# Kernel tuning notes

Measured on AMD Instinct MI355X. Metric: run time of the kernel, lower is better.

## Reference

```python
import jax, jax.numpy as jnp
import numpy as np

N = 50000      # n_nodes
E = 800000     # n_edges (before self-loops)
IN = 256       # in_channels
MID = 512      # mid_channel
MID2 = MID // 2
OUT = 64       # out_channels


def setup_inputs() -> dict:
    key = jax.random.key(0)
    ks = jax.random.split(key, 16)
    def w(k, shape):
        fan_in = shape[0]
        return jax.random.normal(k, shape, jnp.float32) * (1.0 / np.sqrt(fan_in))
    return {
        "node_feature": jax.random.normal(ks[0], (N, IN), jnp.float32),
        "edge_index": jax.random.randint(ks[1], (2, E), 0, N, jnp.int32),
        # GCNConv weights (PyG convention: x @ W, bias added after aggregation)
        "Wg1": w(ks[2], (IN, MID)),   "bg1": jnp.zeros((MID,), jnp.float32),
        "Wg2": w(ks[3], (MID, MID2)), "bg2": jnp.zeros((MID2,), jnp.float32),
        "Wg3": w(ks[4], (MID2, OUT)), "bg3": jnp.zeros((OUT,), jnp.float32),
        # parallel Linear layers
        "Wl1": w(ks[5], (IN, MID)),   "bl1": jnp.zeros((MID,), jnp.float32),
        "Wl2": w(ks[6], (MID, MID2)), "bl2": jnp.zeros((MID2,), jnp.float32),
        "Wl3": w(ks[7], (MID2, OUT)), "bl3": jnp.zeros((OUT,), jnp.float32),
    }


def reference(node_feature, edge_index, Wg1, bg1, Wg2, bg2, Wg3, bg3,
              Wl1, bl1, Wl2, bl2, Wl3, bl3):
    n = node_feature.shape[0]
    # list_add_self_loops: append (i, i) for every node
    loops = jnp.arange(n, dtype=edge_index.dtype)
    src = jnp.concatenate([edge_index[0], loops])
    dst = jnp.concatenate([edge_index[1], loops])
    # symmetric GCN normalization: deg computed on graph with self-loops
    deg = jax.ops.segment_sum(jnp.ones_like(dst, jnp.float32), dst, num_segments=n)
    dis = jax.lax.rsqrt(jnp.maximum(deg, 1.0))  # deg >= 1 thanks to self-loops
    norm = dis[src] * dis[dst]                  # [E'] edge coefficients

    def gcn_conv(x, W, b):
        h = x @ W                                            # [N, F_out]
        msgs = h[src] * norm[:, None]                        # gather + scale
        return jax.ops.segment_sum(msgs, dst, num_segments=n) + b  # scatter-add

    h1 = jax.nn.elu(gcn_conv(node_feature, Wg1, bg1)) + node_feature @ Wl1 + bl1
    h2 = jax.nn.elu(gcn_conv(h1, Wg2, bg2)) + h1 @ Wl2 + bl2
    out = gcn_conv(h2, Wg3, bg3) + h2 @ Wl3 + bl3
    return out
```

## Files before the change

kernel.cpp:

```cpp
#include <hip/hip_runtime.h>
#include <hip/hip_bf16.h>
#include <math.h>

#define IN_CH  256
#define MID    512
#define MID2   256
#define OUT_CH 64

typedef __attribute__((ext_vector_type(8))) short s16x8;
typedef __attribute__((ext_vector_type(8))) unsigned short u16x8;
typedef __attribute__((ext_vector_type(4))) unsigned short u16x4;
typedef __attribute__((ext_vector_type(4))) float f32x4;


__global__ __launch_bounds__(256) void deg_kernel(const int* __restrict__ dst,
                                                  int* __restrict__ cnt, int E) {
  int stride = gridDim.x * blockDim.x;
  for (int e = blockIdx.x * blockDim.x + threadIdx.x; e < E; e += stride)
    atomicAdd(&cnt[dst[e]], 1);
}

__global__ __launch_bounds__(1024) void scan_dis_kernel(const int* __restrict__ cnt,
                                                        int* __restrict__ rowstart,
                                                        float* __restrict__ dis, int N) {
  __shared__ int part[1024];
  int t = threadIdx.x;
  int chunk = (N + 1023) >> 10;
  int lo = t * chunk;
  int hi = lo + chunk; if (hi > N) hi = N; if (lo > N) lo = N;
  int s = 0;
  for (int i = lo; i < hi; ++i) s += cnt[i] + 1;
  part[t] = s;
  __syncthreads();
  for (int off = 1; off < 1024; off <<= 1) {
    int v = (t >= off) ? part[t - off] : 0;
    __syncthreads();
    part[t] += v;
    __syncthreads();
  }
  int base = part[t] - s;
  for (int i = lo; i < hi; ++i) {
    int d = cnt[i] + 1;
    rowstart[i] = base;
    dis[i] = rsqrtf((float)d);
    base += d;
  }
  if (t == 1023) rowstart[N] = part[1023];
}

__global__ __launch_bounds__(256) void fill_adj_kernel(const int* __restrict__ src,
                                                       const int* __restrict__ dst,
                                                       const int* __restrict__ rowstart,
                                                       int* __restrict__ cnt2,
                                                       int* __restrict__ adj,
                                                       int E, int N) {
  int total = E + N;
  int stride = gridDim.x * blockDim.x;
  for (int e = blockIdx.x * blockDim.x + threadIdx.x; e < total; e += stride) {
    int s, d;
    if (e < E) { s = src[e]; d = dst[e]; }
    else       { s = d = e - E; }
    int pos = rowstart[d] + atomicAdd(&cnt2[d], 1);
    adj[pos] = s;
  }
}


__device__ inline unsigned bf16_rne(float v) {
  unsigned u = __float_as_uint(v);
  return (u + 0x7FFFu + ((u >> 16) & 1u)) >> 16;
}

__global__ __launch_bounds__(256) void wsplit_cat(const float* __restrict__ W,
                                                  unsigned short* __restrict__ Th,
                                                  unsigned short* __restrict__ Tl,
                                                  int K, int F, int noff) {
  int idx = blockIdx.x * 256 + threadIdx.x;
  if (idx >= K * F) return;
  int k = idx / F, n = idx - k * F;
  float v = W[idx];
  unsigned h = bf16_rne(v);
  float hf = __uint_as_float(h << 16);
  unsigned l = bf16_rne(v - hf);
  Th[(size_t)(noff + n) * K + k] = (unsigned short)h;
  Tl[(size_t)(noff + n) * K + k] = (unsigned short)l;
}

__global__ __launch_bounds__(256) void split_pair(const float* __restrict__ X,
                                                  unsigned short* __restrict__ Xh,
                                                  unsigned short* __restrict__ Xl,
                                                  int n8) {
  int i = blockIdx.x * 256 + threadIdx.x;
  if (i >= n8) return;
  const float4* xp = (const float4*)X + (size_t)i * 2;
  float4 a = xp[0], b = xp[1];
  float vv[8] = {a.x, a.y, a.z, a.w, b.x, b.y, b.z, b.w};
  u16x8 hv, lv;
  #pragma unroll
  for (int j = 0; j < 8; ++j) {
    unsigned h = bf16_rne(vv[j]);
    float hf = __uint_as_float(h << 16);
    unsigned l = bf16_rne(vv[j] - hf);
    hv[j] = (unsigned short)h;
    lv[j] = (unsigned short)l;
  }
  ((u16x8*)Xh)[i] = hv;
  ((u16x8*)Xl)[i] = lv;
}


template<int MODE>
__global__ __launch_bounds__(256, 2)
void gemm_ps(const unsigned short* __restrict__ Agh, const unsigned short* __restrict__ Agl,
             const unsigned short* __restrict__ Bgh, const unsigned short* __restrict__ Bgl,
             const float* __restrict__ bias,
             const float* __restrict__ C1r, float* __restrict__ C1w,
             unsigned short* __restrict__ O2h, unsigned short* __restrict__ O2l,
             float* __restrict__ O2f,
             int Nrows, int K, int F1) {
  __shared__ unsigned short lds[4 * 128 * 64];
  unsigned short* Ah = lds;
  unsigned short* Al = lds + 8192;
  unsigned short* Bh = lds + 16384;
  unsigned short* Bl = lds + 24576;

  const int tid  = threadIdx.x;
  const int lane = tid & 63;
  const int wid  = tid >> 6;
  const int wr = wid >> 1, wc = wid & 1;
  const int row0 = blockIdx.x * 128;
  const int col0 = blockIdx.y * 128;

  f32x4 acc[4][4] = {};

  const int sr    = tid >> 1;
  const int shalf = (tid & 1) << 5;
  int arow = row0 + sr; if (arow > Nrows - 1) arow = Nrows - 1;
  const unsigned short* Ahb = Agh + (size_t)arow * K + shalf;
  const unsigned short* Alb = Agl + (size_t)arow * K + shalf;
  const unsigned short* Bhb = Bgh + (size_t)(col0 + sr) * K + shalf;
  const unsigned short* Blb = Bgl + (size_t)(col0 + sr) * K + shalf;
  int wslot[4];
  #pragma unroll
  for (int i = 0; i < 4; ++i)
    wslot[i] = sr * 64 + ((((shalf >> 3) + i) ^ (sr & 7)) << 3);

  for (int k0 = 0; k0 < K; k0 += 64) {
    u16x8 rah[4], ral[4], rbh[4], rbl[4];
    #pragma unroll
    for (int i = 0; i < 4; ++i) rah[i] = *(const u16x8*)(Ahb + k0 + i * 8);
    #pragma unroll
    for (int i = 0; i < 4; ++i) ral[i] = *(const u16x8*)(Alb + k0 + i * 8);
    #pragma unroll
    for (int i = 0; i < 4; ++i) rbh[i] = *(const u16x8*)(Bhb + k0 + i * 8);
    #pragma unroll
    for (int i = 0; i < 4; ++i) rbl[i] = *(const u16x8*)(Blb + k0 + i * 8);

    __syncthreads();
    #pragma unroll
    for (int i = 0; i < 4; ++i) {
      *(u16x8*)(Ah + wslot[i]) = rah[i];
      *(u16x8*)(Al + wslot[i]) = ral[i];
      *(u16x8*)(Bh + wslot[i]) = rbh[i];
      *(u16x8*)(Bl + wslot[i]) = rbl[i];
    }
    __syncthreads();

    #pragma unroll
    for (int ks = 0; ks < 2; ++ks) {
      const int sw = ((((ks << 2) + (lane >> 4)) ^ (lane & 7)) << 3);
      s16x8 fah[4], fal[4], fbh[4], fbl[4];
      #pragma unroll
      for (int mi = 0; mi < 4; ++mi) {
        int base = (wr * 64 + mi * 16 + (lane & 15)) * 64 + sw;
        fah[mi] = *(const s16x8*)(Ah + base);
        fal[mi] = *(const s16x8*)(Al + base);
      }
      #pragma unroll
      for (int ni = 0; ni < 4; ++ni) {
        int base = (wc * 64 + ni * 16 + (lane & 15)) * 64 + sw;
        fbh[ni] = *(const s16x8*)(Bh + base);
        fbl[ni] = *(const s16x8*)(Bl + base);
      }
      #pragma unroll
      for (int mi = 0; mi < 4; ++mi)
        #pragma unroll
        for (int ni = 0; ni < 4; ++ni) {
          acc[mi][ni] = __builtin_amdgcn_mfma_f32_16x16x32_bf16(fah[mi], fbh[ni], acc[mi][ni], 0, 0, 0);
          acc[mi][ni] = __builtin_amdgcn_mfma_f32_16x16x32_bf16(fah[mi], fbl[ni], acc[mi][ni], 0, 0, 0);
          acc[mi][ni] = __builtin_amdgcn_mfma_f32_16x16x32_bf16(fal[mi], fbh[ni], acc[mi][ni], 0, 0, 0);
        }
    }
  }

  #pragma unroll
  for (int mi = 0; mi < 4; ++mi) {
    #pragma unroll
    for (int r = 0; r < 4; ++r) {
      int rr = row0 + wr * 64 + mi * 16 + (lane >> 4) * 4 + r;
      if (rr >= Nrows) continue;
      #pragma unroll
      for (int ni = 0; ni < 4; ++ni) {
        int cc = col0 + wc * 64 + ni * 16 + (lane & 15);
        float v = acc[mi][ni][r];
        if (MODE == 0) {
          C1w[(size_t)rr * F1 + cc] = v + bias[cc];
        } else if (MODE == 1) {
          float t = v + bias[cc];
          t = (t > 0.f) ? t : expm1f(t);
          t += C1r[(size_t)rr * F1 + cc];
          size_t idx = (size_t)rr * F1 + cc;
          unsigned h = bf16_rne(t);
          float hf = __uint_as_float(h << 16);
          unsigned l = bf16_rne(t - hf);
          O2h[idx] = (unsigned short)h;
          O2l[idx] = (unsigned short)l;
        } else {
          if (cc < F1) {
            C1w[(size_t)rr * F1 + cc] = v + bias[cc];
          } else {
            size_t idx = (size_t)rr * F1 + (cc - F1);
            if (MODE == 2) O2h[idx] = (unsigned short)bf16_rne(v);
            else           O2f[idx] = v;
          }
        }
      }
    }
  }
}


template<int F>
__global__ __launch_bounds__(256) void agg_split(const unsigned short* __restrict__ H,
                                                 const int* __restrict__ adj,
                                                 const int* __restrict__ rowstart,
                                                 const float* __restrict__ dis,
                                                 unsigned short* __restrict__ Zh,
                                                 unsigned short* __restrict__ Zl, int N) {
  constexpr int VF = F / 64;
  typedef __attribute__((ext_vector_type(VF))) unsigned short uvec;
  int node = (int)((blockIdx.x * blockDim.x + threadIdx.x) >> 6);
  int lane = threadIdx.x & 63;
  if (node >= N) return;
  int e = rowstart[node];
  const int end = rowstart[node + 1];

  float acc[VF] = {};
  const unsigned short* base = H + (size_t)lane * VF;
  for (; e + 4 <= end; e += 4) {
    int s0 = adj[e], s1 = adj[e + 1], s2 = adj[e + 2], s3 = adj[e + 3];
    float w0 = dis[s0], w1 = dis[s1], w2 = dis[s2], w3 = dis[s3];
    uvec v0 = *(const uvec*)(base + (size_t)s0 * F);
    uvec v1 = *(const uvec*)(base + (size_t)s1 * F);
    uvec v2 = *(const uvec*)(base + (size_t)s2 * F);
    uvec v3 = *(const uvec*)(base + (size_t)s3 * F);
    #pragma unroll
    for (int j = 0; j < VF; ++j) {
      acc[j] = fmaf(__uint_as_float((unsigned)v0[j] << 16), w0, acc[j]);
      acc[j] = fmaf(__uint_as_float((unsigned)v1[j] << 16), w1, acc[j]);
      acc[j] = fmaf(__uint_as_float((unsigned)v2[j] << 16), w2, acc[j]);
      acc[j] = fmaf(__uint_as_float((unsigned)v3[j] << 16), w3, acc[j]);
    }
  }
  for (; e < end; ++e) {
    int s = adj[e]; float w = dis[s];
    uvec v = *(const uvec*)(base + (size_t)s * F);
    #pragma unroll
    for (int j = 0; j < VF; ++j)
      acc[j] = fmaf(__uint_as_float((unsigned)v[j] << 16), w, acc[j]);
  }

  float di = dis[node];
  uvec hv, lv;
  #pragma unroll
  for (int j = 0; j < VF; ++j) {
    float val = acc[j] * di;
    unsigned h = bf16_rne(val);
    float hf = __uint_as_float(h << 16);
    unsigned l = bf16_rne(val - hf);
    hv[j] = (unsigned short)h;
    lv[j] = (unsigned short)l;
  }
  *(uvec*)(Zh + (size_t)node * F + lane * VF) = hv;
  *(uvec*)(Zl + (size_t)node * F + lane * VF) = lv;
}

template<int F>
__global__ __launch_bounds__(256) void agg_addsplit(const unsigned short* __restrict__ H,
                                                    const int* __restrict__ adj,
                                                    const int* __restrict__ rowstart,
                                                    const float* __restrict__ dis,
                                                    const float* __restrict__ bias,
                                                    const float* __restrict__ lin,
                                                    unsigned short* __restrict__ Zh,
                                                    unsigned short* __restrict__ Zl, int N) {
  constexpr int VF = F / 64;
  typedef __attribute__((ext_vector_type(VF))) unsigned short uvec;
  int node = (int)((blockIdx.x * blockDim.x + threadIdx.x) >> 6);
  int lane = threadIdx.x & 63;
  if (node >= N) return;
  int e = rowstart[node];
  const int end = rowstart[node + 1];

  float acc[VF] = {};
  const unsigned short* base = H + (size_t)lane * VF;
  for (; e + 4 <= end; e += 4) {
    int s0 = adj[e], s1 = adj[e + 1], s2 = adj[e + 2], s3 = adj[e + 3];
    float w0 = dis[s0], w1 = dis[s1], w2 = dis[s2], w3 = dis[s3];
    uvec v0 = *(const uvec*)(base + (size_t)s0 * F);
    uvec v1 = *(const uvec*)(base + (size_t)s1 * F);
    uvec v2 = *(const uvec*)(base + (size_t)s2 * F);
    uvec v3 = *(const uvec*)(base + (size_t)s3 * F);
    #pragma unroll
    for (int j = 0; j < VF; ++j) {
      acc[j] = fmaf(__uint_as_float((unsigned)v0[j] << 16), w0, acc[j]);
      acc[j] = fmaf(__uint_as_float((unsigned)v1[j] << 16), w1, acc[j]);
      acc[j] = fmaf(__uint_as_float((unsigned)v2[j] << 16), w2, acc[j]);
      acc[j] = fmaf(__uint_as_float((unsigned)v3[j] << 16), w3, acc[j]);
    }
  }
  for (; e < end; ++e) {
    int s = adj[e]; float w = dis[s];
    uvec v = *(const uvec*)(base + (size_t)s * F);
    #pragma unroll
    for (int j = 0; j < VF; ++j)
      acc[j] = fmaf(__uint_as_float((unsigned)v[j] << 16), w, acc[j]);
  }

  float di = dis[node];
  const float* bp = bias + lane * VF;
  const float* lp = lin + (size_t)node * F + lane * VF;
  uvec hv, lv;
  #pragma unroll
  for (int j = 0; j < VF; ++j) {
    float val = fmaf(acc[j], di, bp[j]);
    val = (val > 0.f) ? val : expm1f(val);
    val += lp[j];
    unsigned h = bf16_rne(val);
    float hf = __uint_as_float(h << 16);
    unsigned l = bf16_rne(val - hf);
    hv[j] = (unsigned short)h;
    lv[j] = (unsigned short)l;
  }
  *(uvec*)(Zh + (size_t)node * F + lane * VF) = hv;
  *(uvec*)(Zl + (size_t)node * F + lane * VF) = lv;
}

template<int F>
__global__ __launch_bounds__(256) void agg_f32(const float* __restrict__ H,
                                               const int* __restrict__ adj,
                                               const int* __restrict__ rowstart,
                                               const float* __restrict__ dis,
                                               const float* __restrict__ bias,
                                               float* __restrict__ out, int N) {
  int node = (int)((blockIdx.x * blockDim.x + threadIdx.x) >> 6);
  int lane = threadIdx.x & 63;
  if (node >= N) return;
  int e = rowstart[node];
  const int end = rowstart[node + 1];
  float acc = 0.f;
  for (; e + 4 <= end; e += 4) {
    int s0 = adj[e], s1 = adj[e + 1], s2 = adj[e + 2], s3 = adj[e + 3];
    float w0 = dis[s0], w1 = dis[s1], w2 = dis[s2], w3 = dis[s3];
    float q0 = H[(size_t)s0 * F + lane], q1 = H[(size_t)s1 * F + lane];
    float q2 = H[(size_t)s2 * F + lane], q3 = H[(size_t)s3 * F + lane];
    acc = fmaf(q0, w0, acc); acc = fmaf(q1, w1, acc);
    acc = fmaf(q2, w2, acc); acc = fmaf(q3, w3, acc);
  }
  for (; e < end; ++e) {
    int s = adj[e];
    acc = fmaf(H[(size_t)s * F + lane], dis[s], acc);
  }
  out[(size_t)node * F + lane] += fmaf(acc, dis[node], bias[lane]);
}


static inline char* ws_align(char*& ws, size_t bytes) {
  ws = (char*)(((uintptr_t)ws + 255) & ~(uintptr_t)255);
  char* p = ws;
  ws += bytes;
  return p;
}

extern "C" void kernel_launch(void* const* d_in, const int* in_sizes, int n_in,
                              void* d_out, int out_size, void* d_ws, size_t ws_size,
                              hipStream_t stream) {
  const float* x   = (const float*)d_in[0];
  const int*  eidx = (const int*)d_in[1];
  const float* Wg1 = (const float*)d_in[2];
  const float* bg1 = (const float*)d_in[3];
  const float* Wg2 = (const float*)d_in[4];
  const float* bg2 = (const float*)d_in[5];
  const float* Wg3 = (const float*)d_in[6];
  const float* bg3 = (const float*)d_in[7];
  const float* Wl1 = (const float*)d_in[8];
  const float* bl1 = (const float*)d_in[9];
  const float* Wl2 = (const float*)d_in[10];
  const float* bl2 = (const float*)d_in[11];
  const float* Wl3 = (const float*)d_in[12];
  const float* bl3 = (const float*)d_in[13];

  const int N = in_sizes[0] / IN_CH;
  const int E = in_sizes[1] / 2;
  const int* esrc = eidx;
  const int* edst = eidx + E;

  char* ws = (char*)d_ws;
  unsigned short* xh = (unsigned short*)ws_align(ws, (size_t)N * IN_CH * 2);
  unsigned short* xl = (unsigned short*)ws_align(ws, (size_t)N * IN_CH * 2);
  unsigned short* h1h = xh;
  unsigned short* zh = (unsigned short*)ws_align(ws, (size_t)N * IN_CH * 2);
  unsigned short* zl = (unsigned short*)ws_align(ws, (size_t)N * IN_CH * 2);
  float* h2lin = (float*)zh;
  float* h1lin = (float*)ws_align(ws, (size_t)N * MID * 4);
  unsigned short* Hbf = (unsigned short*)h1lin;
  unsigned short* h2h = (unsigned short*)((char*)h1lin + (size_t)N * MID2 * 2);
  unsigned short* h2l = (unsigned short*)((char*)h1lin + (size_t)N * MID2 * 4);
  float*          Hb3 = (float*)((char*)h1lin + (size_t)N * MID2 * 6);
  unsigned short* h1l = (unsigned short*)ws_align(ws, (size_t)N * MID * 2);
  float* dis      = (float*)ws_align(ws, (size_t)N * 4);
  int*   rowstart = (int*)ws_align(ws, (size_t)(N + 1) * 4);
  int*   cnt      = (int*)ws_align(ws, (size_t)N * 4);
  int*   cnt2     = (int*)ws_align(ws, (size_t)N * 4);
  int*   adj      = (int*)ws_align(ws, (size_t)(E + N) * 4);
  unsigned short* w1h = (unsigned short*)ws_align(ws, (size_t)1024 * IN_CH * 2);
  unsigned short* w1l = (unsigned short*)ws_align(ws, (size_t)1024 * IN_CH * 2);
  unsigned short* w2h = (unsigned short*)ws_align(ws, (size_t)512 * MID * 2);
  unsigned short* w2l = (unsigned short*)ws_align(ws, (size_t)512 * MID * 2);
  unsigned short* w3h = (unsigned short*)ws_align(ws, (size_t)128 * MID2 * 2);
  unsigned short* w3l = (unsigned short*)ws_align(ws, (size_t)128 * MID2 * 2);

  hipMemsetAsync(cnt, 0, (size_t)N * 4, stream);
  hipMemsetAsync(cnt2, 0, (size_t)N * 4, stream);
  deg_kernel<<<1024, 256, 0, stream>>>(edst, cnt, E);
  scan_dis_kernel<<<1, 1024, 0, stream>>>(cnt, rowstart, dis, N);
  fill_adj_kernel<<<2048, 256, 0, stream>>>(esrc, edst, rowstart, cnt2, adj, E, N);

  {
    int n1 = IN_CH * MID, n2 = MID * MID2, n3 = MID2 * OUT_CH;
    wsplit_cat<<<(n1 + 255) / 256, 256, 0, stream>>>(Wl1, w1h, w1l, IN_CH, MID, 0);
    wsplit_cat<<<(n1 + 255) / 256, 256, 0, stream>>>(Wg1, w1h, w1l, IN_CH, MID, MID);
    wsplit_cat<<<(n2 + 255) / 256, 256, 0, stream>>>(Wl2, w2h, w2l, MID, MID2, 0);
    wsplit_cat<<<(n2 + 255) / 256, 256, 0, stream>>>(Wg2, w2h, w2l, MID, MID2, MID2);
    wsplit_cat<<<(n3 + 255) / 256, 256, 0, stream>>>(Wl3, w3h, w3l, MID2, OUT_CH, 0);
    wsplit_cat<<<(n3 + 255) / 256, 256, 0, stream>>>(Wg3, w3h, w3l, MID2, OUT_CH, OUT_CH);
  }

  {
    int n8 = N * IN_CH / 8;
    split_pair<<<(n8 + 255) / 256, 256, 0, stream>>>(x, xh, xl, n8);
  }

  const int aggBlocks = (N + 3) / 4;
  const int rowBlocks = (N + 127) / 128;
  float* outp = (float*)d_out;

  agg_split<IN_CH><<<aggBlocks, 256, 0, stream>>>(xh, adj, rowstart, dis, zh, zl, N);
  dim3 g1(rowBlocks, MID / 128);
  gemm_ps<0><<<g1, 256, 0, stream>>>(xh, xl, w1h, w1l, bl1,
                                     nullptr, h1lin, nullptr, nullptr, nullptr,
                                     N, IN_CH, MID);
  gemm_ps<1><<<g1, 256, 0, stream>>>(zh, zl, w1h + (size_t)MID * IN_CH, w1l + (size_t)MID * IN_CH, bg1,
                                     h1lin, nullptr, h1h, h1l, nullptr,
                                     N, IN_CH, MID);

  dim3 g2(rowBlocks, (2 * MID2) / 128);
  gemm_ps<2><<<g2, 256, 0, stream>>>(h1h, h1l, w2h, w2l, bl2,
                                     nullptr, h2lin, Hbf, nullptr, nullptr,
                                     N, MID, MID2);
  agg_addsplit<MID2><<<aggBlocks, 256, 0, stream>>>(Hbf, adj, rowstart, dis, bg2, h2lin, h2h, h2l, N);

  dim3 g3(rowBlocks, (2 * OUT_CH) / 128);
  gemm_ps<3><<<g3, 256, 0, stream>>>(h2h, h2l, w3h, w3l, bl3,
                                     nullptr, outp, nullptr, nullptr, Hb3,
                                     N, MID2, OUT_CH);
  agg_f32<OUT_CH><<<aggBlocks, 256, 0, stream>>>(Hb3, adj, rowstart, dis, bg3, outp, N);
}
```

Measured before the change: 871.2 us.

## Replace LDS-tiled split-bf16 GEMM with single-wave direct-from-global MFMA kernel

```diff
diff --git a/kernel.cpp b/kernel.cpp
--- a/kernel.cpp
+++ b/kernel.cpp
@@ -9,7 +9,6 @@
 
 typedef __attribute__((ext_vector_type(8))) short s16x8;
 typedef __attribute__((ext_vector_type(8))) unsigned short u16x8;
-typedef __attribute__((ext_vector_type(4))) unsigned short u16x4;
 typedef __attribute__((ext_vector_type(4))) float f32x4;
 
 
@@ -109,99 +108,66 @@
 }
 
 
-template<int MODE>
-__global__ __launch_bounds__(256, 2)
-void gemm_ps(const unsigned short* __restrict__ Agh, const unsigned short* __restrict__ Agl,
+template<int MODE, int KK>
+__global__ __launch_bounds__(64, 2)
+void gemm_dw(const unsigned short* __restrict__ Agh, const unsigned short* __restrict__ Agl,
              const unsigned short* __restrict__ Bgh, const unsigned short* __restrict__ Bgl,
              const float* __restrict__ bias,
              const float* __restrict__ C1r, float* __restrict__ C1w,
              unsigned short* __restrict__ O2h, unsigned short* __restrict__ O2l,
              float* __restrict__ O2f,
-             int Nrows, int K, int F1) {
-  __shared__ unsigned short lds[4 * 128 * 64];
-  unsigned short* Ah = lds;
-  unsigned short* Al = lds + 8192;
-  unsigned short* Bh = lds + 16384;
-  unsigned short* Bl = lds + 24576;
-
-  const int tid  = threadIdx.x;
-  const int lane = tid & 63;
-  const int wid  = tid >> 6;
-  const int wr = wid >> 1, wc = wid & 1;
-  const int row0 = blockIdx.x * 128;
-  const int col0 = blockIdx.y * 128;
+             int Nrows, int F1) {
+  const int lane = threadIdx.x;
+  const int row0 = blockIdx.x * 64;
+  const int col0 = blockIdx.y * 64;
+  const int l15  = lane & 15;
+  const int kgrp = (lane >> 4) << 3;
 
   f32x4 acc[4][4] = {};
 
-  const int sr    = tid >> 1;
-  const int shalf = (tid & 1) << 5;
-  int arow = row0 + sr; if (arow > Nrows - 1) arow = Nrows - 1;
-  const unsigned short* Ahb = Agh + (size_t)arow * K + shalf;
-  const unsigned short* Alb = Agl + (size_t)arow * K + shalf;
-  const unsigned short* Bhb = Bgh + (size_t)(col0 + sr) * K + shalf;
-  const unsigned short* Blb = Bgl + (size_t)(col0 + sr) * K + shalf;
-  int wslot[4];
-  #pragma unroll
-  for (int i = 0; i < 4; ++i)
-    wslot[i] = sr * 64 + ((((shalf >> 3) + i) ^ (sr & 7)) << 3);
-
-  for (int k0 = 0; k0 < K; k0 += 64) {
-    u16x8 rah[4], ral[4], rbh[4], rbl[4];
-    #pragma unroll
-    for (int i = 0; i < 4; ++i) rah[i] = *(const u16x8*)(Ahb + k0 + i * 8);
-    #pragma unroll
-    for (int i = 0; i < 4; ++i) ral[i] = *(const u16x8*)(Alb + k0 + i * 8);
-    #pragma unroll
-    for (int i = 0; i < 4; ++i) rbh[i] = *(const u16x8*)(Bhb + k0 + i * 8);
-    #pragma unroll
-    for (int i = 0; i < 4; ++i) rbl[i] = *(const u16x8*)(Blb + k0 + i * 8);
-
-    __syncthreads();
-    #pragma unroll
-    for (int i = 0; i < 4; ++i) {
-      *(u16x8*)(Ah + wslot[i]) = rah[i];
-      *(u16x8*)(Al + wslot[i]) = ral[i];
-      *(u16x8*)(Bh + wslot[i]) = rbh[i];
-      *(u16x8*)(Bl + wslot[i]) = rbl[i];
+  size_t aoff[4], boff[4];
+  #pragma unroll
+  for (int mi = 0; mi < 4; ++mi) {
+    int r = row0 + mi * 16 + l15;
+    if (r > Nrows - 1) r = Nrows - 1;
+    aoff[mi] = (size_t)r * KK + kgrp;
+  }
+  #pragma unroll
+  for (int ni = 0; ni < 4; ++ni)
+    boff[ni] = (size_t)(col0 + ni * 16 + l15) * KK + kgrp;
+
+  #pragma unroll
+  for (int k0 = 0; k0 < KK; k0 += 32) {
+    s16x8 fah[4], fal[4], fbh[4], fbl[4];
+    #pragma unroll
+    for (int mi = 0; mi < 4; ++mi) {
+      fah[mi] = *(const s16x8*)(Agh + aoff[mi] + k0);
+      fal[mi] = *(const s16x8*)(Agl + aoff[mi] + k0);
     }
-    __syncthreads();
-
-    #pragma unroll
-    for (int ks = 0; ks < 2; ++ks) {
-      const int sw = ((((ks << 2) + (lane >> 4)) ^ (lane & 7)) << 3);
-      s16x8 fah[4], fal[4], fbh[4], fbl[4];
-      #pragma unroll
-      for (int mi = 0; mi < 4; ++mi) {
-        int base = (wr * 64 + mi * 16 + (lane & 15)) * 64 + sw;
-        fah[mi] = *(const s16x8*)(Ah + base);
-        fal[mi] = *(const s16x8*)(Al + base);
-      }
+    #pragma unroll
+    for (int ni = 0; ni < 4; ++ni) {
+      fbh[ni] = *(const s16x8*)(Bgh + boff[ni] + k0);
+      fbl[ni] = *(const s16x8*)(Bgl + boff[ni] + k0);
+    }
+    #pragma unroll
+    for (int mi = 0; mi < 4; ++mi)
       #pragma unroll
       for (int ni = 0; ni < 4; ++ni) {
-        int base = (wc * 64 + ni * 16 + (lane & 15)) * 64 + sw;
-        fbh[ni] = *(const s16x8*)(Bh + base);
-        fbl[ni] = *(const s16x8*)(Bl + base);
+        acc[mi][ni] = __builtin_amdgcn_mfma_f32_16x16x32_bf16(fah[mi], fbh[ni], acc[mi][ni], 0, 0, 0);
+        acc[mi][ni] = __builtin_amdgcn_mfma_f32_16x16x32_bf16(fah[mi], fbl[ni], acc[mi][ni], 0, 0, 0);
+        acc[mi][ni] = __builtin_amdgcn_mfma_f32_16x16x32_bf16(fal[mi], fbh[ni], acc[mi][ni], 0, 0, 0);
       }
-      #pragma unroll
-      for (int mi = 0; mi < 4; ++mi)
-        #pragma unroll
-        for (int ni = 0; ni < 4; ++ni) {
-          acc[mi][ni] = __builtin_amdgcn_mfma_f32_16x16x32_bf16(fah[mi], fbh[ni], acc[mi][ni], 0, 0, 0);
-          acc[mi][ni] = __builtin_amdgcn_mfma_f32_16x16x32_bf16(fah[mi], fbl[ni], acc[mi][ni], 0, 0, 0);
-          acc[mi][ni] = __builtin_amdgcn_mfma_f32_16x16x32_bf16(fal[mi], fbh[ni], acc[mi][ni], 0, 0, 0);
-        }
-    }
   }
 
   #pragma unroll
   for (int mi = 0; mi < 4; ++mi) {
     #pragma unroll
     for (int r = 0; r < 4; ++r) {
-      int rr = row0 + wr * 64 + mi * 16 + (lane >> 4) * 4 + r;
+      int rr = row0 + mi * 16 + (lane >> 4) * 4 + r;
       if (rr >= Nrows) continue;
       #pragma unroll
       for (int ni = 0; ni < 4; ++ni) {
-        int cc = col0 + wc * 64 + ni * 16 + (lane & 15);
+        int cc = col0 + ni * 16 + l15;
         float v = acc[mi][ni][r];
         if (MODE == 0) {
           C1w[(size_t)rr * F1 + cc] = v + bias[cc];
@@ -452,27 +418,28 @@
   }
 
   const int aggBlocks = (N + 3) / 4;
-  const int rowBlocks = (N + 127) / 128;
+  const int rb64 = (N + 63) / 64;
   float* outp = (float*)d_out;
 
   agg_split<IN_CH><<<aggBlocks, 256, 0, stream>>>(xh, adj, rowstart, dis, zh, zl, N);
-  dim3 g1(rowBlocks, MID / 128);
-  gemm_ps<0><<<g1, 256, 0, stream>>>(xh, xl, w1h, w1l, bl1,
-                                     nullptr, h1lin, nullptr, nullptr, nullptr,
-                                     N, IN_CH, MID);
-  gemm_ps<1><<<g1, 256, 0, stream>>>(zh, zl, w1h + (size_t)MID * IN_CH, w1l + (size_t)MID * IN_CH, bg1,
-                                     h1lin, nullptr, h1h, h1l, nullptr,
-                                     N, IN_CH, MID);
-
-  dim3 g2(rowBlocks, (2 * MID2) / 128);
-  gemm_ps<2><<<g2, 256, 0, stream>>>(h1h, h1l, w2h, w2l, bl2,
-                                     nullptr, h2lin, Hbf, nullptr, nullptr,
-                                     N, MID, MID2);
+  dim3 g1(rb64, MID / 64);
+  gemm_dw<0, IN_CH><<<g1, 64, 0, stream>>>(xh, xl, w1h, w1l, bl1,
+                                           nullptr, h1lin, nullptr, nullptr, nullptr,
+                                           N, MID);
+  gemm_dw<1, IN_CH><<<g1, 64, 0, stream>>>(zh, zl,
+                                           w1h + (size_t)MID * IN_CH, w1l + (size_t)MID * IN_CH, bg1,
+                                           h1lin, nullptr, h1h, h1l, nullptr,
+                                           N, MID);
+
+  dim3 g2(rb64, (2 * MID2) / 64);
+  gemm_dw<2, MID><<<g2, 64, 0, stream>>>(h1h, h1l, w2h, w2l, bl2,
+                                         nullptr, h2lin, Hbf, nullptr, nullptr,
+                                         N, MID2);
   agg_addsplit<MID2><<<aggBlocks, 256, 0, stream>>>(Hbf, adj, rowstart, dis, bg2, h2lin, h2h, h2l, N);
 
-  dim3 g3(rowBlocks, (2 * OUT_CH) / 128);
-  gemm_ps<3><<<g3, 256, 0, stream>>>(h2h, h2l, w3h, w3l, bl3,
-                                     nullptr, outp, nullptr, nullptr, Hb3,
-                                     N, MID2, OUT_CH);
+  dim3 g3(rb64, (2 * OUT_CH) / 64);
+  gemm_dw<3, MID2><<<g3, 64, 0, stream>>>(h2h, h2l, w3h, w3l, bl3,
+                                          nullptr, outp, nullptr, nullptr, Hb3,
+                                          N, OUT_CH);
   agg_f32<OUT_CH><<<aggBlocks, 256, 0, stream>>>(Hb3, adj, rowstart, dis, bg3, outp, N);
 }
```

Measured after the change: 1.110 ms. +27.4%, slower.
